# Kernel tuning notes

Measured on AMD Instinct MI355X. Metric: run time of the kernel, lower is better.

The kernel has to match this reference:

```python
import jax, jax.numpy as jnp
import numpy as np

PAD = 32  # integer padding from init_kwargs

def _conv1d_fft(x, weight, bias):
    # x: (B, Cin, L), weight: (Cout, Cin, K), bias: (Cout,)
    B, Cin, L = x.shape
    Cout, _, K = weight.shape
    p = PAD
    padded = (L + 2 * p + 31) & ~31          # round up to multiple of 32
    out_len = 2 * p + L - (K - 1)
    offset = (min(K, L) - 1) // 2 - p
    roll = -((K - 1) // 2) + offset
    # pad kernel to padded length then circularly roll (centers the kernel)
    k_pad = jnp.pad(weight, ((0, 0), (0, 0), (0, padded - K)))
    k_rolled = jnp.roll(k_pad, roll, axis=-1)
    x_fft = jnp.fft.rfft(x, n=padded, axis=-1)          # (B, Cin, F)
    k_fft = jnp.fft.rfft(k_rolled, axis=-1)             # (Cout, Cin, F)
    # multiply-reduce over in_channels == batched complex GEMM over freq bins
    b_fft = jnp.einsum('bif,oif->bof', x_fft, jnp.conj(k_fft))
    # bias enters only the DC bin, scaled by padded length (irfft normalization)
    b_fft = b_fft.at[..., 0].add(bias.astype(b_fft.dtype) * padded)
    b = jnp.fft.irfft(b_fft, n=padded, axis=-1)
    return b[..., :out_len]


def setup_inputs() -> dict:
    key = jax.random.key(0)
    k1, k2, k3 = jax.random.split(key, 3)
    B, Cin, Cout, L, K = 16, 128, 128, 4096, 129
    stdv = 1.0 / np.sqrt(Cin * K)
    x = jax.random.normal(k1, (B, Cin, L), dtype=jnp.float32)
    weight = jax.random.uniform(k2, (Cout, Cin, K), dtype=jnp.float32, minval=-stdv, maxval=stdv)
    bias = jax.random.uniform(k3, (Cout,), dtype=jnp.float32, minval=-stdv, maxval=stdv)
    return {"x": x, "weight": weight, "bias": bias}


def reference(x, weight, bias):
    return _conv1d_fft(x, weight, bias)
```

## Files before the change

kernel.cpp:

```cpp
#include <hip/hip_runtime.h>


typedef _Float16 f16;
typedef _Float16 f16x8 __attribute__((ext_vector_type(8)));
typedef float f32x4 __attribute__((ext_vector_type(4)));

#define NB   16
#define CI   128
#define CO   128
#define LIN  4096
#define KW   129
#define TOUT 4032
#define UPAD 4224
#define XT_BYTES ((size_t)NB * UPAD * CI * 2)

__device__ __forceinline__ void gld16(void* lds, const void* g) {
    __builtin_amdgcn_global_load_lds(
        (const __attribute__((address_space(1))) unsigned int*)g,
        (__attribute__((address_space(3))) unsigned int*)lds,
        16, 0, 0);
}

__global__ __launch_bounds__(256) void xt_prep(const float* __restrict__ x,
                                               f16* __restrict__ xt) {
    __shared__ float tile[128][33];
    const int b  = blockIdx.y;
    const int u0 = blockIdx.x * 32;
    const int l0 = u0 - 32;
    const int tid = threadIdx.x;
    const int col = tid & 31;
    const int cib = tid >> 5;
#pragma unroll
    for (int r = 0; r < 16; ++r) {
        int ci = cib + r * 8;
        int l  = l0 + col;
        float v = 0.f;
        if (l >= 0 && l < LIN) v = x[((size_t)b * CI + ci) * LIN + l];
        tile[ci][col] = v;
    }
    __syncthreads();
#pragma unroll
    for (int it = 0; it < 2; ++it) {
        int idx  = tid + it * 256;
        int ur   = idx >> 4;
        int slot = idx & 15;
        int c    = slot ^ ((u0 + ur) & 7);
        f16x8 v;
#pragma unroll
        for (int j = 0; j < 8; ++j) v[j] = (f16)tile[c * 8 + j][ur];
        *(f16x8*)(&xt[((size_t)b * UPAD + u0 + ur) * CI + slot * 8]) = v;
    }
}

__global__ __launch_bounds__(256) void wt_prep(const float* __restrict__ w,
                                               f16* __restrict__ wt) {
    __shared__ float tile[32][132];
    const int cic = blockIdx.x;
    const int co  = blockIdx.y;
    const int ci0 = cic * 32;
    const int tid = threadIdx.x;
    for (int it = 0; it < 17; ++it) {
        int idx = tid + it * 256;
        if (idx < 32 * 129) {
            int i = idx / 129;
            int m = idx - i * 129;
            tile[i][m] = w[(size_t)co * (CI * KW) + (size_t)(ci0 + i) * KW + m];
        }
    }
    __syncthreads();
    for (int it = 0; it < 3; ++it) {
        int idx = tid + it * 256;
        if (idx < 129 * 4) {
            int m = idx >> 2;
            int c = idx & 3;
            int kk = m * 4 + cic;
            f16x8 v;
#pragma unroll
            for (int j = 0; j < 8; ++j) v[j] = (f16)tile[c * 8 + j][m];
            *(f16x8*)(&wt[((size_t)kk * 128 + co) * 32 + c * 8]) = v;
        }
    }
}

__global__ __launch_bounds__(256, 2) void conv_main(
    const f16* __restrict__ xt, const f16* __restrict__ wt,
    const float* __restrict__ bias, float* __restrict__ out)
{
    extern __shared__ char smem[];
    const int tid  = threadIdx.x;
    const int lane = tid & 63;
    const int wid  = tid >> 6;
    const int l15  = lane & 15;
    const int l4   = lane >> 4;
    const int wco  = (wid >> 1) << 6;
    const int wtt  = (wid & 1) << 6;

    const int tt = blockIdx.x;
    const int b  = blockIdx.y;
    const int u0 = tt << 7;

    const char* xbase = (const char*)xt + ((size_t)b * UPAD + u0) * (CI * 2);
    const char* wbase = (const char*)wt;

    int wrow_off[4];
#pragma unroll
    for (int ct = 0; ct < 4; ++ct)
        wrow_off[ct] = (wco + ct * 16 + l15) * 64 + l4 * 16;

    int brow[4];
#pragma unroll
    for (int st = 0; st < 4; ++st)
        brow[st] = wtt + st * 16 + l15;

    f32x4 acc[4][4];
#pragma unroll
    for (int i = 0; i < 4; ++i)
#pragma unroll
        for (int j = 0; j < 4; ++j)
            acc[i][j] = (f32x4){0.f, 0.f, 0.f, 0.f};

    for (int p = 0; p < 2; ++p) {
        if (p) __syncthreads();
#pragma unroll
        for (int i = 0; i < 8; ++i) {
            int off   = tid * 16 + i * 4096;
            int row   = off >> 7;
            int inrow = off & 127;
            gld16(smem + off, xbase + row * 256 + p * 128 + inrow);
        }
        __syncthreads();

        const char* wp = wbase + p * (2 * 8192);

        f16x8 af[4], an[4];
#pragma unroll
        for (int ct = 0; ct < 4; ++ct)
            af[ct] = *(const f16x8*)(wp + wrow_off[ct]);

#pragma unroll 2
        for (int s = 0; s < 258; ++s) {
            const int sp = (s + 1 < 258) ? s + 1 : 257;
            const int o  = (sp >> 1) * 32768 + (sp & 1) * 8192;
#pragma unroll
            for (int ct = 0; ct < 4; ++ct)
                an[ct] = *(const f16x8*)(wp + o + wrow_off[ct]);

            const int m  = s >> 1;
            const int cl = ((s & 1) << 2) + l4;

            f16x8 bf[4];
#pragma unroll
            for (int st = 0; st < 4; ++st) {
                int row  = brow[st] + m;
                int slot = cl ^ (row & 7);
                bf[st] = *(const f16x8*)(smem + (row << 7) + (slot << 4));
            }
#pragma unroll
            for (int ct = 0; ct < 4; ++ct)
#pragma unroll
                for (int st = 0; st < 4; ++st)
                    acc[ct][st] = __builtin_amdgcn_mfma_f32_16x16x32_f16(
                        af[ct], bf[st], acc[ct][st], 0, 0, 0);
#pragma unroll
            for (int ct = 0; ct < 4; ++ct)
                af[ct] = an[ct];
        }
    }

#pragma unroll
    for (int ct = 0; ct < 4; ++ct) {
#pragma unroll
        for (int r = 0; r < 4; ++r) {
            int co = wco + ct * 16 + l4 * 4 + r;
            float bv = bias[co];
            float* orow = out + ((size_t)b * CO + co) * TOUT;
#pragma unroll
            for (int st = 0; st < 4; ++st) {
                int t = u0 + wtt + st * 16 + l15;
                if (t < TOUT) orow[t] = acc[ct][st][r] + bv;
            }
        }
    }
}

extern "C" void kernel_launch(void* const* d_in, const int* in_sizes, int n_in,
                              void* d_out, int out_size, void* d_ws, size_t ws_size,
                              hipStream_t stream) {
    const float* x    = (const float*)d_in[0];
    const float* w    = (const float*)d_in[1];
    const float* bias = (const float*)d_in[2];
    float* out = (float*)d_out;

    f16* xt = (f16*)d_ws;
    f16* wt = (f16*)((char*)d_ws + XT_BYTES);

    xt_prep<<<dim3(UPAD / 32, NB), 256, 0, stream>>>(x, xt);
    wt_prep<<<dim3(4, CO), 256, 0, stream>>>(w, wt);
    conv_main<<<dim3(32, NB), 256, 32768, stream>>>(xt, wt, bias, out);
}
```

Measured before the change: 365.5 us.

## Stage weights through a triple-buffered LDS ring with chunked x layout

```diff
diff --git a/kernel.cpp b/kernel.cpp
--- a/kernel.cpp
+++ b/kernel.cpp
@@ -12,7 +12,8 @@
 #define KW   129
 #define TOUT 4032
 #define UPAD 4224
-#define XT_BYTES ((size_t)NB * UPAD * CI * 2)
+#define XT_BYTES ((size_t)NB * 2 * 8 * UPAD * 16)
+#define WLDS 32768
 
 __device__ __forceinline__ void gld16(void* lds, const void* g) {
     __builtin_amdgcn_global_load_lds(
@@ -41,14 +42,14 @@
     __syncthreads();
 #pragma unroll
     for (int it = 0; it < 2; ++it) {
-        int idx  = tid + it * 256;
-        int ur   = idx >> 4;
-        int slot = idx & 15;
-        int c    = slot ^ ((u0 + ur) & 7);
+        int idx   = tid + it * 256;
+        int chunk = idx >> 5;
+        int ur    = idx & 31;
         f16x8 v;
 #pragma unroll
-        for (int j = 0; j < 8; ++j) v[j] = (f16)tile[c * 8 + j][ur];
-        *(f16x8*)(&xt[((size_t)b * UPAD + u0 + ur) * CI + slot * 8]) = v;
+        for (int j = 0; j < 8; ++j) v[j] = (f16)tile[chunk * 8 + j][ur];
+        size_t unit = ((size_t)b * 16 + chunk) * UPAD + (u0 + ur);
+        *(f16x8*)(&xt[unit * 8]) = v;
     }
 }
 
@@ -77,7 +78,7 @@
             f16x8 v;
 #pragma unroll
             for (int j = 0; j < 8; ++j) v[j] = (f16)tile[c * 8 + j][m];
-            *(f16x8*)(&wt[((size_t)kk * 128 + co) * 32 + c * 8]) = v;
+            *(f16x8*)(&wt[(size_t)kk * 4096 + c * 1024 + co * 8]) = v;
         }
     }
 }
@@ -99,18 +100,20 @@
     const int b  = blockIdx.y;
     const int u0 = tt << 7;
 
-    const char* xbase = (const char*)xt + ((size_t)b * UPAD + u0) * (CI * 2);
     const char* wbase = (const char*)wt;
-
-    int wrow_off[4];
+    char* wring = smem + WLDS;
+
+    int aoff[4];
 #pragma unroll
     for (int ct = 0; ct < 4; ++ct)
-        wrow_off[ct] = (wco + ct * 16 + l15) * 64 + l4 * 16;
-
-    int brow[4];
+        aoff[ct] = l4 * 2048 + (wco + ct * 16 + l15) * 16;
+    int qb[2];
+#pragma unroll
+    for (int q = 0; q < 2; ++q) qb[q] = (q * 4 + l4) * 4096;
+    int xoff[4];
 #pragma unroll
     for (int st = 0; st < 4; ++st)
-        brow[st] = wtt + st * 16 + l15;
+        xoff[st] = (wtt + st * 16 + l15) * 16;
 
     f32x4 acc[4][4];
 #pragma unroll
@@ -119,52 +122,94 @@
         for (int j = 0; j < 4; ++j)
             acc[i][j] = (f32x4){0.f, 0.f, 0.f, 0.f};
 
+    f16x8 afA[2][4], bfA[2][4], afB[2][4], bfB[2][4];
+
     for (int p = 0; p < 2; ++p) {
-        if (p) __syncthreads();
-#pragma unroll
-        for (int i = 0; i < 8; ++i) {
-            int off   = tid * 16 + i * 4096;
-            int row   = off >> 7;
-            int inrow = off & 127;
-            gld16(smem + off, xbase + row * 256 + p * 128 + inrow);
-        }
-        __syncthreads();
-
-        const char* wp = wbase + p * (2 * 8192);
-
-        f16x8 af[4], an[4];
-#pragma unroll
-        for (int ct = 0; ct < 4; ++ct)
-            af[ct] = *(const f16x8*)(wp + wrow_off[ct]);
-
-#pragma unroll 2
-        for (int s = 0; s < 258; ++s) {
-            const int sp = (s + 1 < 258) ? s + 1 : 257;
-            const int o  = (sp >> 1) * 32768 + (sp & 1) * 8192;
+        const int pbase = 2 * p;
+
+        if (p) {
+            asm volatile("s_waitcnt lgkmcnt(0)" ::: "memory");
+            __builtin_amdgcn_s_barrier();
+        }
+        const char* xph = (const char*)xt +
+            (((size_t)b * 16 + p * 8) * UPAD + u0) * 16;
+#pragma unroll
+        for (int i = 0; i < 8; ++i)
+            gld16(smem + tid * 16 + i * 4096, xph + (size_t)i * (UPAD * 16) + tid * 16);
+        {
+            const char* ws0 = wbase + (size_t)pbase * 8192;
+            gld16(wring + tid * 16,         ws0 + tid * 16);
+            gld16(wring + 4096 + tid * 16,  ws0 + 4096 + tid * 16);
+            gld16(wring + 8192 + tid * 16,  ws0 + 8192 + tid * 16);
+            gld16(wring + 12288 + tid * 16, ws0 + 12288 + tid * 16);
+            const char* ws1 = wbase + (size_t)(4 + pbase) * 8192;
+            gld16(wring + 16384 + tid * 16, ws1 + tid * 16);
+            gld16(wring + 20480 + tid * 16, ws1 + 4096 + tid * 16);
+            gld16(wring + 24576 + tid * 16, ws1 + 8192 + tid * 16);
+            gld16(wring + 28672 + tid * 16, ws1 + 12288 + tid * 16);
+        }
+        asm volatile("s_waitcnt vmcnt(4)" ::: "memory");
+        __builtin_amdgcn_s_barrier();
+        __builtin_amdgcn_sched_barrier(0);
+
+#pragma unroll
+        for (int q = 0; q < 2; ++q) {
 #pragma unroll
             for (int ct = 0; ct < 4; ++ct)
-                an[ct] = *(const f16x8*)(wp + o + wrow_off[ct]);
-
-            const int m  = s >> 1;
-            const int cl = ((s & 1) << 2) + l4;
-
-            f16x8 bf[4];
-#pragma unroll
-            for (int st = 0; st < 4; ++st) {
-                int row  = brow[st] + m;
-                int slot = cl ^ (row & 7);
-                bf[st] = *(const f16x8*)(smem + (row << 7) + (slot << 4));
+                afA[q][ct] = *(const f16x8*)(wring + q * 8192 + aoff[ct]);
+#pragma unroll
+            for (int st = 0; st < 4; ++st)
+                bfA[q][st] = *(const f16x8*)(smem + qb[q] + xoff[st]);
+        }
+
+        int rpF = 1, rpD = 2;
+
+        auto body = [&](int t, f16x8 (&afC)[2][4], f16x8 (&bfC)[2][4],
+                               f16x8 (&afN)[2][4], f16x8 (&bfN)[2][4]) {
+            const bool issue = (t + 2 <= 128);
+            if (issue) {
+                const char* wsrc = wbase + (size_t)(4 * (t + 2) + pbase) * 8192;
+                char* dst = wring + rpD * 16384;
+                gld16(dst + tid * 16,         wsrc + tid * 16);
+                gld16(dst + 4096 + tid * 16,  wsrc + 4096 + tid * 16);
+                gld16(dst + 8192 + tid * 16,  wsrc + 8192 + tid * 16);
+                gld16(dst + 12288 + tid * 16, wsrc + 12288 + tid * 16);
+                asm volatile("s_waitcnt vmcnt(4)" ::: "memory");
+            } else {
+                asm volatile("s_waitcnt vmcnt(0)" ::: "memory");
             }
-#pragma unroll
-            for (int ct = 0; ct < 4; ++ct)
-#pragma unroll
-                for (int st = 0; st < 4; ++st)
-                    acc[ct][st] = __builtin_amdgcn_mfma_f32_16x16x32_f16(
-                        af[ct], bf[st], acc[ct][st], 0, 0, 0);
-#pragma unroll
-            for (int ct = 0; ct < 4; ++ct)
-                af[ct] = an[ct];
-        }
+            __builtin_amdgcn_s_barrier();
+            __builtin_amdgcn_sched_barrier(0);
+            if (t + 1 <= 128) {
+                const int mn = (t + 1) * 16;
+                const char* wl = wring + rpF * 16384;
+#pragma unroll
+                for (int q = 0; q < 2; ++q) {
+#pragma unroll
+                    for (int ct = 0; ct < 4; ++ct)
+                        afN[q][ct] = *(const f16x8*)(wl + q * 8192 + aoff[ct]);
+#pragma unroll
+                    for (int st = 0; st < 4; ++st)
+                        bfN[q][st] = *(const f16x8*)(smem + qb[q] + xoff[st] + mn);
+                }
+            }
+#pragma unroll
+            for (int q = 0; q < 2; ++q)
+#pragma unroll
+                for (int ct = 0; ct < 4; ++ct)
+#pragma unroll
+                    for (int st = 0; st < 4; ++st)
+                        acc[ct][st] = __builtin_amdgcn_mfma_f32_16x16x32_f16(
+                            afC[q][ct], bfC[q][st], acc[ct][st], 0, 0, 0);
+            rpF = (rpF == 2) ? 0 : rpF + 1;
+            rpD = (rpD == 2) ? 0 : rpD + 1;
+        };
+
+        for (int t2 = 0; t2 < 128; t2 += 2) {
+            body(t2,     afA, bfA, afB, bfB);
+            body(t2 + 1, afB, bfB, afA, bfA);
+        }
+        body(128, afA, bfA, afB, bfB);
     }
 
 #pragma unroll
@@ -196,5 +241,5 @@
 
     xt_prep<<<dim3(UPAD / 32, NB), 256, 0, stream>>>(x, xt);
     wt_prep<<<dim3(4, CO), 256, 0, stream>>>(w, wt);
-    conv_main<<<dim3(32, NB), 256, 32768, stream>>>(xt, wt, bias, out);
-}
+    conv_main<<<dim3(32, NB), 256, 81920, stream>>>(xt, wt, bias, out);
+}
```

Result: faster. 310.2 us (-15.1%).
